# Performance work log

Hardware: AMD Instinct MI355X
Metric: run time of the kernel (lower is better)

Reference implementation:

```python
import jax, jax.numpy as jnp
import numpy as np

N, E = 50000, 800000
DIN, DH, DOUT = 128, 128, 64


def setup_inputs() -> dict:
    key = jax.random.key(0)
    k = jax.random.split(key, 6)
    node_features = jax.random.normal(k[0], (N, DIN), dtype=jnp.float32)
    edge_src = jax.random.randint(k[1], (E,), 0, N)
    edge_dst = jax.random.randint(k[2], (E,), 0, N)
    # Glorot-ish init for the two GCNConv weight matrices, zero bias (PyG default bias=True)
    W1 = jax.random.normal(k[3], (DIN, DH), dtype=jnp.float32) * (1.0 / np.sqrt(DIN))
    b1 = jnp.zeros((DH,), dtype=jnp.float32)
    W2 = jax.random.normal(k[4], (DH, DOUT), dtype=jnp.float32) * (1.0 / np.sqrt(DH))
    b2 = jnp.zeros((DOUT,), dtype=jnp.float32)
    return {"node_features": node_features, "edge_src": edge_src, "edge_dst": edge_dst,
            "W1": W1, "b1": b1, "W2": W2, "b2": b2}


def gcn_conv(x, W, b, src, dst, n):
    """PyG GCNConv: add self-loops, symmetric D^-1/2 (A+I) D^-1/2 normalization."""
    xw = x @ W  # [n, d_out]
    loops = jnp.arange(n, dtype=src.dtype)
    s = jnp.concatenate([src, loops])  # edges + self-loops
    d = jnp.concatenate([dst, loops])
    deg = jax.ops.segment_sum(jnp.ones_like(d, dtype=xw.dtype), d, num_segments=n)
    dinv = jnp.where(deg > 0, jax.lax.rsqrt(deg), 0.0)
    norm = dinv[s] * dinv[d]  # [E + n]
    msg = xw[s] * norm[:, None]  # gather + scale (memory-bound)
    out = jax.ops.segment_sum(msg, d, num_segments=n)  # scatter-add
    return out + b


def reference(node_features, edge_src, edge_dst, W1, b1, W2, b2):
    n = node_features.shape[0]
    h = gcn_conv(node_features, W1, b1, edge_src, edge_dst, n)
    h = jax.nn.relu(h)  # dropout omitted (inference / eval mode)
    h = gcn_conv(h, W2, b2, edge_src, edge_dst, n)
    # EdgePredictor: per-edge dot product of endpoint representations
    score = jnp.sum(h[edge_src] * h[edge_dst], axis=-1)  # [E]
    return score
```

## Files before the change

### kernel.cpp

```cpp
#include <hip/hip_runtime.h>
#include <hip/hip_bf16.h>
#include <type_traits>


#define DIN 128
#define DH  128
#define DOUT 64
#define CAP 8192

typedef __attribute__((ext_vector_type(8))) short short8;
typedef __attribute__((ext_vector_type(4))) float floatx4;

__device__ inline float2 bf2_to_f2(unsigned u) {
    union { unsigned i; float f; } a, b;
    a.i = u << 16;
    b.i = u & 0xffff0000u;
    return make_float2(a.f, b.f);
}
__device__ inline float bf_to_f(unsigned short u) {
    union { unsigned i; float f; } a;
    a.i = ((unsigned)u) << 16;
    return a.f;
}
__device__ inline unsigned short f_to_bf(float f) {
    union { float f; unsigned i; } v; v.f = f;
    unsigned r = v.i + 0x7fffu + ((v.i >> 16) & 1u);
    return (unsigned short)(r >> 16);
}

__global__ __launch_bounds__(256) void bucket_count_kernel(const int* __restrict__ dst,
                                                           int* __restrict__ gcnt,
                                                           int E, int nbuck) {
    __shared__ int hist[256];
    int t = threadIdx.x;
    hist[t] = 0;
    __syncthreads();
    int base = blockIdx.x * 4096 + t;
#pragma unroll
    for (int it = 0; it < 16; ++it) {
        int e = base + it * 256;
        if (e < E) atomicAdd(&hist[dst[e] >> 8], 1);
    }
    __syncthreads();
    if (t < nbuck && hist[t]) atomicAdd(&gcnt[t], hist[t]);
}

__global__ __launch_bounds__(256) void scan_buckets_kernel(const int* __restrict__ gcnt,
                                                           int* __restrict__ gbase,
                                                           int* __restrict__ gcursor,
                                                           int* __restrict__ row_ptr,
                                                           int nbuck, int N, int E) {
    __shared__ int lds[256];
    int t = threadIdx.x;
    int v = (t < nbuck) ? gcnt[t] : 0;
    lds[t] = v;
    __syncthreads();
    for (int off = 1; off < 256; off <<= 1) {
        int u = (t >= off) ? lds[t - off] : 0;
        __syncthreads();
        lds[t] += u;
        __syncthreads();
    }
    int ex = lds[t] - v;
    if (t < nbuck) { gbase[t] = ex; gcursor[t] = ex; }
    if (t == 0) { gbase[nbuck] = E; row_ptr[N] = E; }
}

__global__ __launch_bounds__(256) void bucket_place_kernel(const int* __restrict__ src,
                                                           const int* __restrict__ dst,
                                                           int* __restrict__ gcursor,
                                                           uint2* __restrict__ tmp,
                                                           int E, int nbuck) {
    __shared__ int hist[256];
    __shared__ int cur[256];
    int t = threadIdx.x;
    hist[t] = 0;
    __syncthreads();
    int base = blockIdx.x * 4096 + t;
    int d[16];
#pragma unroll
    for (int it = 0; it < 16; ++it) {
        int e = base + it * 256;
        d[it] = (e < E) ? dst[e] : -1;
        if (d[it] >= 0) atomicAdd(&hist[d[it] >> 8], 1);
    }
    __syncthreads();
    if (t < nbuck && hist[t]) cur[t] = atomicAdd(&gcursor[t], hist[t]);
    __syncthreads();
#pragma unroll
    for (int it = 0; it < 16; ++it) {
        int e = base + it * 256;
        if (d[it] >= 0) {
            int r = atomicAdd(&cur[d[it] >> 8], 1);
            tmp[r] = make_uint2((unsigned)src[e] | ((unsigned)(d[it] & 255) << 16),
                                (unsigned)e);
        }
    }
}

__global__ __launch_bounds__(256) void bucket_csr_kernel(const uint2* __restrict__ tmp,
                                                         const int* __restrict__ gbase,
                                                         int* __restrict__ row_ptr,
                                                         float* __restrict__ dinv,
                                                         int* __restrict__ col,
                                                         int* __restrict__ eidx, int N) {
    __shared__ int hist[256], cur[256], pfx[256];
    __shared__ unsigned ebuf[CAP];
    __shared__ unsigned ibuf[CAP];
    __shared__ unsigned ssrc[CAP];
    __shared__ unsigned sidx[CAP];
    int b = blockIdx.x, t = threadIdx.x;
    int beg = gbase[b], end = gbase[b + 1];
    int size = end - beg;
    if (size > CAP) size = CAP;
    hist[t] = 0;
    __syncthreads();
    for (int i = t; i < size; i += 256) {
        uint2 e = tmp[beg + i];
        ebuf[i] = e.x;
        ibuf[i] = e.y;
        atomicAdd(&hist[e.x >> 16], 1);
    }
    __syncthreads();
    int v = hist[t];
    pfx[t] = v;
    __syncthreads();
    for (int off = 1; off < 256; off <<= 1) {
        int u = (t >= off) ? pfx[t - off] : 0;
        __syncthreads();
        pfx[t] += u;
        __syncthreads();
    }
    int ex = pfx[t] - v;
    cur[t] = ex;
    int node = b * 256 + t;
    if (node < N) {
        row_ptr[node] = beg + ex;
        dinv[node] = rsqrtf((float)(v + 1));
    }
    __syncthreads();
    for (int i = t; i < size; i += 256) {
        int r = atomicAdd(&cur[ebuf[i] >> 16], 1);
        ssrc[r] = ebuf[i] & 0xffffu;
        sidx[r] = ibuf[i];
    }
    __syncthreads();
    for (int i = t; i < size; i += 256) {
        col[beg + i]  = (int)ssrc[i];
        eidx[beg + i] = (int)sidx[i];
    }
}

template <int COLS, typename XT>
__global__ __launch_bounds__(256) void mfma_gemm_kernel(const XT* __restrict__ X,
                                                        const float* __restrict__ W,
                                                        const float* __restrict__ dinv,
                                                        unsigned short* __restrict__ Y,
                                                        int nrows) {
    constexpr int KP = 136;
    __shared__ unsigned short Xs[128 * KP];
    __shared__ unsigned short Wt[COLS * KP];
    int tid = threadIdx.x;
    int row0 = blockIdx.x * 128;

    if constexpr (std::is_same_v<XT, float>) {
#pragma unroll
        for (int it = 0; it < 16; ++it) {
            int idx = it * 256 + tid;
            int r = idx >> 5;
            int c4 = (idx & 31) * 4;
            int gr = row0 + r; if (gr >= nrows) gr = nrows - 1;
            float4 v = *(const float4*)(X + (size_t)gr * 128 + c4);
            ushort4 p;
            p.x = f_to_bf(v.x); p.y = f_to_bf(v.y);
            p.z = f_to_bf(v.z); p.w = f_to_bf(v.w);
            *(ushort4*)&Xs[r * KP + c4] = p;
        }
    } else {
#pragma unroll
        for (int it = 0; it < 8; ++it) {
            int idx = it * 256 + tid;
            int r = idx >> 4;
            int c8 = (idx & 15) * 8;
            int gr = row0 + r; if (gr >= nrows) gr = nrows - 1;
            uint4 v = *(const uint4*)(X + (size_t)gr * 128 + c8);
            *(uint4*)&Xs[r * KP + c8] = v;
        }
    }
#pragma unroll
    for (int it = 0; it < COLS / 8; ++it) {
        int idx = it * 256 + tid;
        int n = idx >> 5;
        int k4 = (idx & 31) * 4;
        ushort4 p;
        p.x = f_to_bf(W[(size_t)(k4 + 0) * COLS + n]);
        p.y = f_to_bf(W[(size_t)(k4 + 1) * COLS + n]);
        p.z = f_to_bf(W[(size_t)(k4 + 2) * COLS + n]);
        p.w = f_to_bf(W[(size_t)(k4 + 3) * COLS + n]);
        *(ushort4*)&Wt[n * KP + k4] = p;
    }
    __syncthreads();

    constexpr int CT = COLS / 16;
    int wv = tid >> 6, lane = tid & 63;
    int lr = lane & 15;
    int lk = (lane >> 4) * 8;
    int rw = wv * 32;

    floatx4 acc[2][CT];
#pragma unroll
    for (int rt = 0; rt < 2; ++rt)
#pragma unroll
        for (int ct = 0; ct < CT; ++ct) acc[rt][ct] = (floatx4){0.f, 0.f, 0.f, 0.f};

#pragma unroll
    for (int kk = 0; kk < 128; kk += 32) {
        short8 a[2], b[CT];
#pragma unroll
        for (int rt = 0; rt < 2; ++rt)
            a[rt] = *(const short8*)&Xs[(rw + rt * 16 + lr) * KP + kk + lk];
#pragma unroll
        for (int ct = 0; ct < CT; ++ct)
            b[ct] = *(const short8*)&Wt[(ct * 16 + lr) * KP + kk + lk];
#pragma unroll
        for (int rt = 0; rt < 2; ++rt)
#pragma unroll
            for (int ct = 0; ct < CT; ++ct)
                acc[rt][ct] = __builtin_amdgcn_mfma_f32_16x16x32_bf16(
                    a[rt], b[ct], acc[rt][ct], 0, 0, 0);
    }

#pragma unroll
    for (int rt = 0; rt < 2; ++rt) {
#pragma unroll
        for (int i = 0; i < 4; ++i) {
            int grow = row0 + rw + rt * 16 + (lane >> 4) * 4 + i;
            if (grow >= nrows) continue;
            float dv = dinv[grow];
#pragma unroll
            for (int ct = 0; ct < CT; ++ct)
                Y[(size_t)grow * COLS + ct * 16 + lr] =
                    f_to_bf(acc[rt][ct][i] * dv);
        }
    }
}

template <int D, bool RELU>
__global__ __launch_bounds__(256) void agg_kernel(const unsigned short* __restrict__ y,
                                                  const int* __restrict__ row_ptr,
                                                  const int* __restrict__ col,
                                                  const float* __restrict__ dinv,
                                                  const float* __restrict__ bias,
                                                  unsigned short* __restrict__ out, int n) {
    constexpr int V = D / 64;
    int w = (blockIdx.x * 256 + threadIdx.x) >> 6;
    int lane = threadIdx.x & 63;
    if (w >= n) return;
    float acc[V];
    if constexpr (V == 2) {
        float2 t = bf2_to_f2(*(const unsigned*)(y + (size_t)w * D + lane * 2));
        acc[0] = t.x; acc[1] = t.y;
    } else {
        acc[0] = bf_to_f(y[(size_t)w * D + lane]);
    }
    int beg = row_ptr[w], end = row_ptr[w + 1];
    int i = beg;
    for (; i + 8 <= end; i += 8) {
        int s[8];
#pragma unroll
        for (int u = 0; u < 8; ++u) s[u] = col[i + u];
        if constexpr (V == 2) {
            unsigned tv[8];
#pragma unroll
            for (int u = 0; u < 8; ++u)
                tv[u] = *(const unsigned*)(y + (size_t)s[u] * D + lane * 2);
#pragma unroll
            for (int u = 0; u < 8; ++u) {
                float2 f = bf2_to_f2(tv[u]);
                acc[0] += f.x; acc[1] += f.y;
            }
        } else {
            unsigned short tv[8];
#pragma unroll
            for (int u = 0; u < 8; ++u) tv[u] = y[(size_t)s[u] * D + lane];
#pragma unroll
            for (int u = 0; u < 8; ++u) acc[0] += bf_to_f(tv[u]);
        }
    }
    for (; i < end; ++i) {
        int s = col[i];
        if constexpr (V == 2) {
            float2 f = bf2_to_f2(*(const unsigned*)(y + (size_t)s * D + lane * 2));
            acc[0] += f.x; acc[1] += f.y;
        } else {
            acc[0] += bf_to_f(y[(size_t)s * D + lane]);
        }
    }
    float dv = dinv[w];
    if constexpr (V == 2) {
        float r0 = fmaf(dv, acc[0], bias[lane * 2]);
        float r1 = fmaf(dv, acc[1], bias[lane * 2 + 1]);
        if (RELU) { r0 = fmaxf(r0, 0.f); r1 = fmaxf(r1, 0.f); }
        unsigned pk = (unsigned)f_to_bf(r0) | ((unsigned)f_to_bf(r1) << 16);
        *(unsigned*)(out + (size_t)w * D + lane * 2) = pk;
    } else {
        float r = fmaf(dv, acc[0], bias[lane]);
        if (RELU) r = fmaxf(r, 0.f);
        out[(size_t)w * D + lane] = f_to_bf(r);
    }
}

__global__ __launch_bounds__(256) void score_csr_kernel(const unsigned short* __restrict__ h2,
                                                        const int* __restrict__ row_ptr,
                                                        const int* __restrict__ col,
                                                        const int* __restrict__ eidx,
                                                        float* __restrict__ out, int n) {
    int w = (blockIdx.x * 256 + threadIdx.x) >> 6;
    int lane = threadIdx.x & 63;
    if (w >= n) return;
    int q = lane & 7;
    uint4 hd = *(const uint4*)(h2 + (size_t)w * 64 + q * 8);
    float d0[8];
    { float2 f;
      f = bf2_to_f2(hd.x); d0[0] = f.x; d0[1] = f.y;
      f = bf2_to_f2(hd.y); d0[2] = f.x; d0[3] = f.y;
      f = bf2_to_f2(hd.z); d0[4] = f.x; d0[5] = f.y;
      f = bf2_to_f2(hd.w); d0[6] = f.x; d0[7] = f.y; }
    int beg = row_ptr[w], end = row_ptr[w + 1];
    int g = lane >> 3;
    for (int i = beg; i < end; i += 8) {
        int ei = i + g;
        bool ok = ei < end;
        int s = ok ? col[ei] : 0;
        uint4 hs = *(const uint4*)(h2 + (size_t)s * 64 + q * 8);
        float v = 0.f;
        float2 f;
        f = bf2_to_f2(hs.x); v = fmaf(d0[0], f.x, v); v = fmaf(d0[1], f.y, v);
        f = bf2_to_f2(hs.y); v = fmaf(d0[2], f.x, v); v = fmaf(d0[3], f.y, v);
        f = bf2_to_f2(hs.z); v = fmaf(d0[4], f.x, v); v = fmaf(d0[5], f.y, v);
        f = bf2_to_f2(hs.w); v = fmaf(d0[6], f.x, v); v = fmaf(d0[7], f.y, v);
        v += __shfl_xor(v, 4);
        v += __shfl_xor(v, 2);
        v += __shfl_xor(v, 1);
        if (ok && q == 0) out[eidx[ei]] = v;
    }
}

extern "C" void kernel_launch(void* const* d_in, const int* in_sizes, int n_in,
                              void* d_out, int out_size, void* d_ws, size_t ws_size,
                              hipStream_t stream) {
    const float* X   = (const float*)d_in[0];
    const int*   src = (const int*)d_in[1];
    const int*   dst = (const int*)d_in[2];
    const float* W1  = (const float*)d_in[3];
    const float* b1  = (const float*)d_in[4];
    const float* W2  = (const float*)d_in[5];
    const float* b2  = (const float*)d_in[6];
    float* score = (float*)d_out;

    const int N = in_sizes[0] / DIN;
    const int E = in_sizes[1];
    const int nbuck = (N + 255) / 256;
    const int EB = (E + 4095) / 4096;

    auto align = [](size_t x) { return (x + 255) & ~(size_t)255; };
    char* p = (char*)d_ws;
    int*   gcnt    = (int*)p;               p += align(256 * 4);
    int*   gbase   = (int*)p;               p += align(257 * 4);
    int*   gcursor = (int*)p;               p += align(256 * 4);
    int*   row_ptr = (int*)p;               p += align((size_t)(N + 1) * 4);
    float* dinv    = (float*)p;             p += align((size_t)N * 4);
    int*   col     = (int*)p;               p += align((size_t)E * 4);
    int*   eidx    = (int*)p;               p += align((size_t)E * 4);
    uint2* tmp     = (uint2*)p;             p += align((size_t)E * 8);
    unsigned short* y1 = (unsigned short*)p; p += align((size_t)N * DH * 2);
    unsigned short* h1 = (unsigned short*)p; p += align((size_t)N * DH * 2);
    unsigned short* y2 = y1;
    unsigned short* h2 = y1 + (size_t)N * DOUT;

    hipMemsetAsync(gcnt, 0, 256 * 4, stream);

    bucket_count_kernel<<<EB, 256, 0, stream>>>(dst, gcnt, E, nbuck);
    scan_buckets_kernel<<<1, 256, 0, stream>>>(gcnt, gbase, gcursor, row_ptr, nbuck, N, E);
    bucket_place_kernel<<<EB, 256, 0, stream>>>(src, dst, gcursor, tmp, E, nbuck);
    bucket_csr_kernel<<<nbuck, 256, 0, stream>>>(tmp, gbase, row_ptr, dinv, col, eidx, N);

    int gemm_blocks = (N + 127) / 128;
    mfma_gemm_kernel<DH, float><<<gemm_blocks, 256, 0, stream>>>(X, W1, dinv, y1, N);

    int agg_blocks = (N + 3) / 4;
    agg_kernel<DH, true><<<agg_blocks, 256, 0, stream>>>(y1, row_ptr, col, dinv, b1, h1, N);

    mfma_gemm_kernel<DOUT, unsigned short><<<gemm_blocks, 256, 0, stream>>>(h1, W2, dinv, y2, N);
    agg_kernel<DOUT, false><<<agg_blocks, 256, 0, stream>>>(y2, row_ptr, col, dinv, b2, h2, N);

    score_csr_kernel<<<agg_blocks, 256, 0, stream>>>(h2, row_ptr, col, eidx, score, N);
}
```

Before: 255.9 us.

## Merge CSR front-end and agg2+score into cooperative kernels with grid sync

The count, scan and placement CSR-building kernels and the memset are merged into one cooperative kernel. It uses per-chunk histograms and grid.sync, so the global atomics on the counters and two launches go away. The second aggregation and the edge-score kernel are fused into one persistent cooperative kernel, with a grid-wide barrier between them. This cuts launch gaps, but the front end now runs on only 256 blocks and the fused kernel uses a fixed grid of 1024 blocks, which may lower parallelism. It also relies on NCH=196 chunks being enough for E.

```diff
diff --git a/kernel.cpp b/kernel.cpp
--- a/kernel.cpp
+++ b/kernel.cpp
@@ -1,12 +1,16 @@
 #include <hip/hip_runtime.h>
 #include <hip/hip_bf16.h>
+#include <hip/hip_cooperative_groups.h>
 #include <type_traits>
+
+namespace cg = cooperative_groups;
 
 
 #define DIN 128
 #define DH  128
 #define DOUT 64
 #define CAP 8192
+#define NCH 196
 
 typedef __attribute__((ext_vector_type(8))) short short8;
 typedef __attribute__((ext_vector_type(4))) float floatx4;
@@ -28,73 +32,81 @@
     return (unsigned short)(r >> 16);
 }
 
-__global__ __launch_bounds__(256) void bucket_count_kernel(const int* __restrict__ dst,
-                                                           int* __restrict__ gcnt,
-                                                           int E, int nbuck) {
-    __shared__ int hist[256];
-    int t = threadIdx.x;
-    hist[t] = 0;
-    __syncthreads();
-    int base = blockIdx.x * 4096 + t;
-#pragma unroll
-    for (int it = 0; it < 16; ++it) {
-        int e = base + it * 256;
-        if (e < E) atomicAdd(&hist[dst[e] >> 8], 1);
-    }
-    __syncthreads();
-    if (t < nbuck && hist[t]) atomicAdd(&gcnt[t], hist[t]);
-}
-
-__global__ __launch_bounds__(256) void scan_buckets_kernel(const int* __restrict__ gcnt,
-                                                           int* __restrict__ gbase,
-                                                           int* __restrict__ gcursor,
-                                                           int* __restrict__ row_ptr,
-                                                           int nbuck, int N, int E) {
-    __shared__ int lds[256];
-    int t = threadIdx.x;
-    int v = (t < nbuck) ? gcnt[t] : 0;
-    lds[t] = v;
-    __syncthreads();
-    for (int off = 1; off < 256; off <<= 1) {
-        int u = (t >= off) ? lds[t - off] : 0;
-        __syncthreads();
-        lds[t] += u;
-        __syncthreads();
-    }
-    int ex = lds[t] - v;
-    if (t < nbuck) { gbase[t] = ex; gcursor[t] = ex; }
-    if (t == 0) { gbase[nbuck] = E; row_ptr[N] = E; }
-}
-
-__global__ __launch_bounds__(256) void bucket_place_kernel(const int* __restrict__ src,
-                                                           const int* __restrict__ dst,
-                                                           int* __restrict__ gcursor,
-                                                           uint2* __restrict__ tmp,
-                                                           int E, int nbuck) {
+__global__ __launch_bounds__(256) void csr_front_kernel(
+    const int* __restrict__ src, const int* __restrict__ dst,
+    int* __restrict__ gcnt2, int* __restrict__ gbase, int* __restrict__ gcursor,
+    int* __restrict__ row_ptr, uint2* __restrict__ tmp,
+    int N, int E, int nbuck, int nchunk) {
+    cg::grid_group grid = cg::this_grid();
     __shared__ int hist[256];
     __shared__ int cur[256];
-    int t = threadIdx.x;
-    hist[t] = 0;
-    __syncthreads();
-    int base = blockIdx.x * 4096 + t;
-    int d[16];
-#pragma unroll
-    for (int it = 0; it < 16; ++it) {
-        int e = base + it * 256;
-        d[it] = (e < E) ? dst[e] : -1;
-        if (d[it] >= 0) atomicAdd(&hist[d[it] >> 8], 1);
-    }
-    __syncthreads();
-    if (t < nbuck && hist[t]) cur[t] = atomicAdd(&gcursor[t], hist[t]);
-    __syncthreads();
-#pragma unroll
-    for (int it = 0; it < 16; ++it) {
-        int e = base + it * 256;
-        if (d[it] >= 0) {
-            int r = atomicAdd(&cur[d[it] >> 8], 1);
-            tmp[r] = make_uint2((unsigned)src[e] | ((unsigned)(d[it] & 255) << 16),
-                                (unsigned)e);
-        }
+    int t = threadIdx.x, b = blockIdx.x, G = gridDim.x;
+
+    for (int c = b; c < nchunk; c += G) {
+        hist[t] = 0;
+        __syncthreads();
+        int base = c * 4096 + t;
+#pragma unroll
+        for (int it = 0; it < 16; ++it) {
+            int e = base + it * 256;
+            if (e < E) atomicAdd(&hist[dst[e] >> 8], 1);
+        }
+        __syncthreads();
+        gcnt2[c * 256 + t] = hist[t];
+        __syncthreads();
+    }
+    grid.sync();
+
+    if (b == 0) {
+        int s0 = 0, s1 = 0, s2 = 0, s3 = 0;
+        int c = 0;
+        for (; c + 4 <= nchunk; c += 4) {
+            s0 += gcnt2[(c + 0) * 256 + t];
+            s1 += gcnt2[(c + 1) * 256 + t];
+            s2 += gcnt2[(c + 2) * 256 + t];
+            s3 += gcnt2[(c + 3) * 256 + t];
+        }
+        for (; c < nchunk; ++c) s0 += gcnt2[c * 256 + t];
+        int v = s0 + s1 + s2 + s3;
+        hist[t] = v;
+        __syncthreads();
+        for (int off = 1; off < 256; off <<= 1) {
+            int u = (t >= off) ? hist[t - off] : 0;
+            __syncthreads();
+            hist[t] += u;
+            __syncthreads();
+        }
+        int ex = hist[t] - v;
+        gbase[t] = ex;
+        gcursor[t] = ex;
+        if (t == 0) { gbase[nbuck] = E; row_ptr[N] = E; }
+    }
+    grid.sync();
+
+    for (int c = b; c < nchunk; c += G) {
+        hist[t] = 0;
+        __syncthreads();
+        int base = c * 4096 + t;
+        int d[16];
+#pragma unroll
+        for (int it = 0; it < 16; ++it) {
+            int e = base + it * 256;
+            d[it] = (e < E) ? dst[e] : -1;
+            if (d[it] >= 0) atomicAdd(&hist[d[it] >> 8], 1);
+        }
+        __syncthreads();
+        if (hist[t]) cur[t] = atomicAdd(&gcursor[t], hist[t]);
+        __syncthreads();
+#pragma unroll
+        for (int it = 0; it < 16; ++it) {
+            int e = base + it * 256;
+            if (d[it] >= 0) {
+                int r = atomicAdd(&cur[d[it] >> 8], 1);
+                tmp[r] = make_uint2((unsigned)src[e] | ((unsigned)(d[it] & 255) << 16),
+                                    (unsigned)e);
+            }
+        }
+        __syncthreads();
     }
 }
 
@@ -245,23 +257,19 @@
     }
 }
 
-template <int D, bool RELU>
-__global__ __launch_bounds__(256) void agg_kernel(const unsigned short* __restrict__ y,
-                                                  const int* __restrict__ row_ptr,
-                                                  const int* __restrict__ col,
-                                                  const float* __restrict__ dinv,
-                                                  const float* __restrict__ bias,
-                                                  unsigned short* __restrict__ out, int n) {
-    constexpr int V = D / 64;
+__global__ __launch_bounds__(256) void agg1_kernel(const unsigned short* __restrict__ y,
+                                                   const int* __restrict__ row_ptr,
+                                                   const int* __restrict__ col,
+                                                   const float* __restrict__ dinv,
+                                                   const float* __restrict__ bias,
+                                                   unsigned short* __restrict__ out, int n) {
     int w = (blockIdx.x * 256 + threadIdx.x) >> 6;
     int lane = threadIdx.x & 63;
     if (w >= n) return;
-    float acc[V];
-    if constexpr (V == 2) {
-        float2 t = bf2_to_f2(*(const unsigned*)(y + (size_t)w * D + lane * 2));
-        acc[0] = t.x; acc[1] = t.y;
-    } else {
-        acc[0] = bf_to_f(y[(size_t)w * D + lane]);
+    float acc0, acc1;
+    {
+        float2 t = bf2_to_f2(*(const unsigned*)(y + (size_t)w * 128 + lane * 2));
+        acc0 = t.x; acc1 = t.y;
     }
     int beg = row_ptr[w], end = row_ptr[w + 1];
     int i = beg;
@@ -269,80 +277,84 @@
         int s[8];
 #pragma unroll
         for (int u = 0; u < 8; ++u) s[u] = col[i + u];
-        if constexpr (V == 2) {
-            unsigned tv[8];
-#pragma unroll
-            for (int u = 0; u < 8; ++u)
-                tv[u] = *(const unsigned*)(y + (size_t)s[u] * D + lane * 2);
-#pragma unroll
-            for (int u = 0; u < 8; ++u) {
-                float2 f = bf2_to_f2(tv[u]);
-                acc[0] += f.x; acc[1] += f.y;
-            }
-        } else {
+        unsigned tv[8];
+#pragma unroll
+        for (int u = 0; u < 8; ++u)
+            tv[u] = *(const unsigned*)(y + (size_t)s[u] * 128 + lane * 2);
+#pragma unroll
+        for (int u = 0; u < 8; ++u) {
+            float2 f = bf2_to_f2(tv[u]);
+            acc0 += f.x; acc1 += f.y;
+        }
+    }
+    for (; i < end; ++i) {
+        float2 f = bf2_to_f2(*(const unsigned*)(y + (size_t)col[i] * 128 + lane * 2));
+        acc0 += f.x; acc1 += f.y;
+    }
+    float dv = dinv[w];
+    float r0 = fmaxf(fmaf(dv, acc0, bias[lane * 2]), 0.f);
+    float r1 = fmaxf(fmaf(dv, acc1, bias[lane * 2 + 1]), 0.f);
+    unsigned pk = (unsigned)f_to_bf(r0) | ((unsigned)f_to_bf(r1) << 16);
+    *(unsigned*)(out + (size_t)w * 128 + lane * 2) = pk;
+}
+
+__global__ __launch_bounds__(256) void agg2_score_kernel(
+    const unsigned short* __restrict__ y2, const int* __restrict__ row_ptr,
+    const int* __restrict__ col, const int* __restrict__ eidx,
+    const float* __restrict__ dinv, const float* __restrict__ bias,
+    unsigned short* __restrict__ h2, float* __restrict__ out, int n) {
+    cg::grid_group grid = cg::this_grid();
+    int gw = (blockIdx.x * 256 + threadIdx.x) >> 6;
+    int NW = (gridDim.x * 256) >> 6;
+    int lane = threadIdx.x & 63;
+
+    for (int w = gw; w < n; w += NW) {
+        float acc = bf_to_f(y2[(size_t)w * 64 + lane]);
+        int beg = row_ptr[w], end = row_ptr[w + 1];
+        int i = beg;
+        for (; i + 8 <= end; i += 8) {
+            int s[8];
+#pragma unroll
+            for (int u = 0; u < 8; ++u) s[u] = col[i + u];
             unsigned short tv[8];
 #pragma unroll
-            for (int u = 0; u < 8; ++u) tv[u] = y[(size_t)s[u] * D + lane];
-#pragma unroll
-            for (int u = 0; u < 8; ++u) acc[0] += bf_to_f(tv[u]);
-        }
-    }
-    for (; i < end; ++i) {
-        int s = col[i];
-        if constexpr (V == 2) {
-            float2 f = bf2_to_f2(*(const unsigned*)(y + (size_t)s * D + lane * 2));
-            acc[0] += f.x; acc[1] += f.y;
-        } else {
-            acc[0] += bf_to_f(y[(size_t)s * D + lane]);
-        }
-    }
-    float dv = dinv[w];
-    if constexpr (V == 2) {
-        float r0 = fmaf(dv, acc[0], bias[lane * 2]);
-        float r1 = fmaf(dv, acc[1], bias[lane * 2 + 1]);
-        if (RELU) { r0 = fmaxf(r0, 0.f); r1 = fmaxf(r1, 0.f); }
-        unsigned pk = (unsigned)f_to_bf(r0) | ((unsigned)f_to_bf(r1) << 16);
-        *(unsigned*)(out + (size_t)w * D + lane * 2) = pk;
-    } else {
-        float r = fmaf(dv, acc[0], bias[lane]);
-        if (RELU) r = fmaxf(r, 0.f);
-        out[(size_t)w * D + lane] = f_to_bf(r);
-    }
-}
-
-__global__ __launch_bounds__(256) void score_csr_kernel(const unsigned short* __restrict__ h2,
-                                                        const int* __restrict__ row_ptr,
-                                                        const int* __restrict__ col,
-                                                        const int* __restrict__ eidx,
-                                                        float* __restrict__ out, int n) {
-    int w = (blockIdx.x * 256 + threadIdx.x) >> 6;
-    int lane = threadIdx.x & 63;
-    if (w >= n) return;
+            for (int u = 0; u < 8; ++u) tv[u] = y2[(size_t)s[u] * 64 + lane];
+#pragma unroll
+            for (int u = 0; u < 8; ++u) acc += bf_to_f(tv[u]);
+        }
+        for (; i < end; ++i) acc += bf_to_f(y2[(size_t)col[i] * 64 + lane]);
+        float r = fmaf(dinv[w], acc, bias[lane]);
+        h2[(size_t)w * 64 + lane] = f_to_bf(r);
+    }
+    grid.sync();
+
     int q = lane & 7;
-    uint4 hd = *(const uint4*)(h2 + (size_t)w * 64 + q * 8);
-    float d0[8];
-    { float2 f;
-      f = bf2_to_f2(hd.x); d0[0] = f.x; d0[1] = f.y;
-      f = bf2_to_f2(hd.y); d0[2] = f.x; d0[3] = f.y;
-      f = bf2_to_f2(hd.z); d0[4] = f.x; d0[5] = f.y;
-      f = bf2_to_f2(hd.w); d0[6] = f.x; d0[7] = f.y; }
-    int beg = row_ptr[w], end = row_ptr[w + 1];
     int g = lane >> 3;
-    for (int i = beg; i < end; i += 8) {
-        int ei = i + g;
-        bool ok = ei < end;
-        int s = ok ? col[ei] : 0;
-        uint4 hs = *(const uint4*)(h2 + (size_t)s * 64 + q * 8);
-        float v = 0.f;
-        float2 f;
-        f = bf2_to_f2(hs.x); v = fmaf(d0[0], f.x, v); v = fmaf(d0[1], f.y, v);
-        f = bf2_to_f2(hs.y); v = fmaf(d0[2], f.x, v); v = fmaf(d0[3], f.y, v);
-        f = bf2_to_f2(hs.z); v = fmaf(d0[4], f.x, v); v = fmaf(d0[5], f.y, v);
-        f = bf2_to_f2(hs.w); v = fmaf(d0[6], f.x, v); v = fmaf(d0[7], f.y, v);
-        v += __shfl_xor(v, 4);
-        v += __shfl_xor(v, 2);
-        v += __shfl_xor(v, 1);
-        if (ok && q == 0) out[eidx[ei]] = v;
+    for (int w = gw; w < n; w += NW) {
+        uint4 hd = *(const uint4*)(h2 + (size_t)w * 64 + q * 8);
+        float d0[8];
+        { float2 f;
+          f = bf2_to_f2(hd.x); d0[0] = f.x; d0[1] = f.y;
+          f = bf2_to_f2(hd.y); d0[2] = f.x; d0[3] = f.y;
+          f = bf2_to_f2(hd.z); d0[4] = f.x; d0[5] = f.y;
+          f = bf2_to_f2(hd.w); d0[6] = f.x; d0[7] = f.y; }
+        int beg = row_ptr[w], end = row_ptr[w + 1];
+        for (int i = beg; i < end; i += 8) {
+            int ei = i + g;
+            bool ok = ei < end;
+            int s = ok ? col[ei] : 0;
+            uint4 hs = *(const uint4*)(h2 + (size_t)s * 64 + q * 8);
+            float v = 0.f;
+            float2 f;
+            f = bf2_to_f2(hs.x); v = fmaf(d0[0], f.x, v); v = fmaf(d0[1], f.y, v);
+            f = bf2_to_f2(hs.y); v = fmaf(d0[2], f.x, v); v = fmaf(d0[3], f.y, v);
+            f = bf2_to_f2(hs.z); v = fmaf(d0[4], f.x, v); v = fmaf(d0[5], f.y, v);
+            f = bf2_to_f2(hs.w); v = fmaf(d0[6], f.x, v); v = fmaf(d0[7], f.y, v);
+            v += __shfl_xor(v, 4);
+            v += __shfl_xor(v, 2);
+            v += __shfl_xor(v, 1);
+            if (ok && q == 0) out[eidx[ei]] = v;
+        }
     }
 }
 
@@ -358,14 +370,14 @@
     const float* b2  = (const float*)d_in[6];
     float* score = (float*)d_out;
 
-    const int N = in_sizes[0] / DIN;
-    const int E = in_sizes[1];
-    const int nbuck = (N + 255) / 256;
-    const int EB = (E + 4095) / 4096;
+    int N = in_sizes[0] / DIN;
+    int E = in_sizes[1];
+    int nbuck = (N + 255) / 256;
+    int nchunk = (E + 4095) / 4096;
 
     auto align = [](size_t x) { return (x + 255) & ~(size_t)255; };
     char* p = (char*)d_ws;
-    int*   gcnt    = (int*)p;               p += align(256 * 4);
+    int*   gcnt2   = (int*)p;               p += align((size_t)NCH * 256 * 4);
     int*   gbase   = (int*)p;               p += align(257 * 4);
     int*   gcursor = (int*)p;               p += align(256 * 4);
     int*   row_ptr = (int*)p;               p += align((size_t)(N + 1) * 4);
@@ -378,21 +390,29 @@
     unsigned short* y2 = y1;
     unsigned short* h2 = y1 + (size_t)N * DOUT;
 
-    hipMemsetAsync(gcnt, 0, 256 * 4, stream);
-
-    bucket_count_kernel<<<EB, 256, 0, stream>>>(dst, gcnt, E, nbuck);
-    scan_buckets_kernel<<<1, 256, 0, stream>>>(gcnt, gbase, gcursor, row_ptr, nbuck, N, E);
-    bucket_place_kernel<<<EB, 256, 0, stream>>>(src, dst, gcursor, tmp, E, nbuck);
+    {
+        void* argsA[] = {(void*)&src, (void*)&dst, (void*)&gcnt2, (void*)&gbase,
+                         (void*)&gcursor, (void*)&row_ptr, (void*)&tmp,
+                         (void*)&N, (void*)&E, (void*)&nbuck, (void*)&nchunk};
+        hipLaunchCooperativeKernel((const void*)csr_front_kernel, dim3(256),
+                                   dim3(256), argsA, 0, stream);
+    }
+
     bucket_csr_kernel<<<nbuck, 256, 0, stream>>>(tmp, gbase, row_ptr, dinv, col, eidx, N);
 
     int gemm_blocks = (N + 127) / 128;
     mfma_gemm_kernel<DH, float><<<gemm_blocks, 256, 0, stream>>>(X, W1, dinv, y1, N);
 
     int agg_blocks = (N + 3) / 4;
-    agg_kernel<DH, true><<<agg_blocks, 256, 0, stream>>>(y1, row_ptr, col, dinv, b1, h1, N);
+    agg1_kernel<<<agg_blocks, 256, 0, stream>>>(y1, row_ptr, col, dinv, b1, h1, N);
 
     mfma_gemm_kernel<DOUT, unsigned short><<<gemm_blocks, 256, 0, stream>>>(h1, W2, dinv, y2, N);
-    agg_kernel<DOUT, false><<<agg_blocks, 256, 0, stream>>>(y2, row_ptr, col, dinv, b2, h2, N);
-
-    score_csr_kernel<<<agg_blocks, 256, 0, stream>>>(h2, row_ptr, col, eidx, score, N);
-}
+
+    {
+        void* argsB[] = {(void*)&y2, (void*)&row_ptr, (void*)&col, (void*)&eidx,
+                         (void*)&dinv, (void*)&b2, (void*)&h2, (void*)&score,
+                         (void*)&N};
+        hipLaunchCooperativeKernel((const void*)agg2_score_kernel, dim3(1024),
+                                   dim3(256), argsB, 0, stream);
+    }
+}
```

New measurement: 492.3 us. +92.4%, slower.

## Use fixed-capacity bucket slots to drop the count and scan kernels in CSR build

Applied to the files above, without the earlier changes.

Each 256-node destination bucket now gets a fixed slot of CAP entries in the temp, col and eidx arrays. This lets the place kernel claim positions straight from a zeroed per-bucket cursor. The bucket_count and scan_buckets kernels go away, along with the extra pass over dst and two launches. Rows are now described by separate row_beg/row_end arrays, so the aggregation and score kernels load two index arrays instead of one. The layout uses more workspace and silently drops edges if a bucket ever exceeds CAP.

```diff
diff --git a/kernel.cpp b/kernel.cpp
--- a/kernel.cpp
+++ b/kernel.cpp
@@ -28,49 +28,10 @@
     return (unsigned short)(r >> 16);
 }
 
-__global__ __launch_bounds__(256) void bucket_count_kernel(const int* __restrict__ dst,
-                                                           int* __restrict__ gcnt,
-                                                           int E, int nbuck) {
-    __shared__ int hist[256];
-    int t = threadIdx.x;
-    hist[t] = 0;
-    __syncthreads();
-    int base = blockIdx.x * 4096 + t;
-#pragma unroll
-    for (int it = 0; it < 16; ++it) {
-        int e = base + it * 256;
-        if (e < E) atomicAdd(&hist[dst[e] >> 8], 1);
-    }
-    __syncthreads();
-    if (t < nbuck && hist[t]) atomicAdd(&gcnt[t], hist[t]);
-}
-
-__global__ __launch_bounds__(256) void scan_buckets_kernel(const int* __restrict__ gcnt,
-                                                           int* __restrict__ gbase,
-                                                           int* __restrict__ gcursor,
-                                                           int* __restrict__ row_ptr,
-                                                           int nbuck, int N, int E) {
-    __shared__ int lds[256];
-    int t = threadIdx.x;
-    int v = (t < nbuck) ? gcnt[t] : 0;
-    lds[t] = v;
-    __syncthreads();
-    for (int off = 1; off < 256; off <<= 1) {
-        int u = (t >= off) ? lds[t - off] : 0;
-        __syncthreads();
-        lds[t] += u;
-        __syncthreads();
-    }
-    int ex = lds[t] - v;
-    if (t < nbuck) { gbase[t] = ex; gcursor[t] = ex; }
-    if (t == 0) { gbase[nbuck] = E; row_ptr[N] = E; }
-}
-
-__global__ __launch_bounds__(256) void bucket_place_kernel(const int* __restrict__ src,
-                                                           const int* __restrict__ dst,
-                                                           int* __restrict__ gcursor,
-                                                           uint2* __restrict__ tmp,
-                                                           int E, int nbuck) {
+__global__ __launch_bounds__(256) void place_kernel(const int* __restrict__ src,
+                                                    const int* __restrict__ dst,
+                                                    int* __restrict__ cursor,
+                                                    uint2* __restrict__ tmp, int E) {
     __shared__ int hist[256];
     __shared__ int cur[256];
     int t = threadIdx.x;
@@ -85,22 +46,26 @@
         if (d[it] >= 0) atomicAdd(&hist[d[it] >> 8], 1);
     }
     __syncthreads();
-    if (t < nbuck && hist[t]) cur[t] = atomicAdd(&gcursor[t], hist[t]);
+    if (hist[t]) cur[t] = atomicAdd(&cursor[t], hist[t]);
     __syncthreads();
 #pragma unroll
     for (int it = 0; it < 16; ++it) {
         int e = base + it * 256;
         if (d[it] >= 0) {
-            int r = atomicAdd(&cur[d[it] >> 8], 1);
-            tmp[r] = make_uint2((unsigned)src[e] | ((unsigned)(d[it] & 255) << 16),
-                                (unsigned)e);
+            int bkt = d[it] >> 8;
+            int r = atomicAdd(&cur[bkt], 1);
+            if (r < CAP)
+                tmp[(size_t)bkt * CAP + r] =
+                    make_uint2((unsigned)src[e] | ((unsigned)(d[it] & 255) << 16),
+                               (unsigned)e);
         }
     }
 }
 
 __global__ __launch_bounds__(256) void bucket_csr_kernel(const uint2* __restrict__ tmp,
-                                                         const int* __restrict__ gbase,
-                                                         int* __restrict__ row_ptr,
+                                                         const int* __restrict__ cursor,
+                                                         int* __restrict__ row_beg,
+                                                         int* __restrict__ row_end,
                                                          float* __restrict__ dinv,
                                                          int* __restrict__ col,
                                                          int* __restrict__ eidx, int N) {
@@ -110,13 +75,13 @@
     __shared__ unsigned ssrc[CAP];
     __shared__ unsigned sidx[CAP];
     int b = blockIdx.x, t = threadIdx.x;
-    int beg = gbase[b], end = gbase[b + 1];
-    int size = end - beg;
+    int size = cursor[b];
     if (size > CAP) size = CAP;
+    size_t rbase = (size_t)b * CAP;
     hist[t] = 0;
     __syncthreads();
     for (int i = t; i < size; i += 256) {
-        uint2 e = tmp[beg + i];
+        uint2 e = tmp[rbase + i];
         ebuf[i] = e.x;
         ibuf[i] = e.y;
         atomicAdd(&hist[e.x >> 16], 1);
@@ -135,7 +100,8 @@
     cur[t] = ex;
     int node = b * 256 + t;
     if (node < N) {
-        row_ptr[node] = beg + ex;
+        row_beg[node] = (int)rbase + ex;
+        row_end[node] = (int)rbase + ex + v;
         dinv[node] = rsqrtf((float)(v + 1));
     }
     __syncthreads();
@@ -146,8 +112,8 @@
     }
     __syncthreads();
     for (int i = t; i < size; i += 256) {
-        col[beg + i]  = (int)ssrc[i];
-        eidx[beg + i] = (int)sidx[i];
+        col[rbase + i]  = (int)ssrc[i];
+        eidx[rbase + i] = (int)sidx[i];
     }
 }
 
@@ -247,7 +213,8 @@
 
 template <int D, bool RELU>
 __global__ __launch_bounds__(256) void agg_kernel(const unsigned short* __restrict__ y,
-                                                  const int* __restrict__ row_ptr,
+                                                  const int* __restrict__ row_beg,
+                                                  const int* __restrict__ row_end,
                                                   const int* __restrict__ col,
                                                   const float* __restrict__ dinv,
                                                   const float* __restrict__ bias,
@@ -263,7 +230,7 @@
     } else {
         acc[0] = bf_to_f(y[(size_t)w * D + lane]);
     }
-    int beg = row_ptr[w], end = row_ptr[w + 1];
+    int beg = row_beg[w], end = row_end[w];
     int i = beg;
     for (; i + 8 <= end; i += 8) {
         int s[8];
@@ -311,7 +278,8 @@
 }
 
 __global__ __launch_bounds__(256) void score_csr_kernel(const unsigned short* __restrict__ h2,
-                                                        const int* __restrict__ row_ptr,
+                                                        const int* __restrict__ row_beg,
+                                                        const int* __restrict__ row_end,
                                                         const int* __restrict__ col,
                                                         const int* __restrict__ eidx,
                                                         float* __restrict__ out, int n) {
@@ -326,7 +294,7 @@
       f = bf2_to_f2(hd.y); d0[2] = f.x; d0[3] = f.y;
       f = bf2_to_f2(hd.z); d0[4] = f.x; d0[5] = f.y;
       f = bf2_to_f2(hd.w); d0[6] = f.x; d0[7] = f.y; }
-    int beg = row_ptr[w], end = row_ptr[w + 1];
+    int beg = row_beg[w], end = row_end[w];
     int g = lane >> 3;
     for (int i = beg; i < end; i += 8) {
         int ei = i + g;
@@ -365,34 +333,35 @@
 
     auto align = [](size_t x) { return (x + 255) & ~(size_t)255; };
     char* p = (char*)d_ws;
-    int*   gcnt    = (int*)p;               p += align(256 * 4);
-    int*   gbase   = (int*)p;               p += align(257 * 4);
-    int*   gcursor = (int*)p;               p += align(256 * 4);
-    int*   row_ptr = (int*)p;               p += align((size_t)(N + 1) * 4);
+    int*   cursor  = (int*)p;               p += align(256 * 4);
+    int*   row_beg = (int*)p;               p += align((size_t)N * 4);
+    int*   row_end = (int*)p;               p += align((size_t)N * 4);
     float* dinv    = (float*)p;             p += align((size_t)N * 4);
-    int*   col     = (int*)p;               p += align((size_t)E * 4);
-    int*   eidx    = (int*)p;               p += align((size_t)E * 4);
-    uint2* tmp     = (uint2*)p;             p += align((size_t)E * 8);
+    int*   col     = (int*)p;               p += align((size_t)nbuck * CAP * 4);
+    int*   eidx    = (int*)p;               p += align((size_t)nbuck * CAP * 4);
+    uint2* tmp     = (uint2*)p;             p += align((size_t)nbuck * CAP * 8);
     unsigned short* y1 = (unsigned short*)p; p += align((size_t)N * DH * 2);
     unsigned short* h1 = (unsigned short*)p; p += align((size_t)N * DH * 2);
     unsigned short* y2 = y1;
     unsigned short* h2 = y1 + (size_t)N * DOUT;
 
-    hipMemsetAsync(gcnt, 0, 256 * 4, stream);
-
-    bucket_count_kernel<<<EB, 256, 0, stream>>>(dst, gcnt, E, nbuck);
-    scan_buckets_kernel<<<1, 256, 0, stream>>>(gcnt, gbase, gcursor, row_ptr, nbuck, N, E);
-    bucket_place_kernel<<<EB, 256, 0, stream>>>(src, dst, gcursor, tmp, E, nbuck);
-    bucket_csr_kernel<<<nbuck, 256, 0, stream>>>(tmp, gbase, row_ptr, dinv, col, eidx, N);
+    hipMemsetAsync(cursor, 0, 256 * 4, stream);
+
+    place_kernel<<<EB, 256, 0, stream>>>(src, dst, cursor, tmp, E);
+    bucket_csr_kernel<<<nbuck, 256, 0, stream>>>(tmp, cursor, row_beg, row_end,
+                                                 dinv, col, eidx, N);
 
     int gemm_blocks = (N + 127) / 128;
     mfma_gemm_kernel<DH, float><<<gemm_blocks, 256, 0, stream>>>(X, W1, dinv, y1, N);
 
     int agg_blocks = (N + 3) / 4;
-    agg_kernel<DH, true><<<agg_blocks, 256, 0, stream>>>(y1, row_ptr, col, dinv, b1, h1, N);
+    agg_kernel<DH, true><<<agg_blocks, 256, 0, stream>>>(y1, row_beg, row_end,
+                                                         col, dinv, b1, h1, N);
 
     mfma_gemm_kernel<DOUT, unsigned short><<<gemm_blocks, 256, 0, stream>>>(h1, W2, dinv, y2, N);
-    agg_kernel<DOUT, false><<<agg_blocks, 256, 0, stream>>>(y2, row_ptr, col, dinv, b2, h2, N);
-
-    score_csr_kernel<<<agg_blocks, 256, 0, stream>>>(h2, row_ptr, col, eidx, score, N);
-}
+    agg_kernel<DOUT, false><<<agg_blocks, 256, 0, stream>>>(y2, row_beg, row_end,
+                                                            col, dinv, b2, h2, N);
+
+    score_csr_kernel<<<agg_blocks, 256, 0, stream>>>(h2, row_beg, row_end,
+                                                     col, eidx, score, N);
+}
```

Measured after the change: 246.5 us. -3.7%, faster.
